# Kernel optimization log

Measured on AMD Instinct MI355X. Metric: run time of the kernel, lower is better.

Reference implementation:

```python
import jax, jax.numpy as jnp
import numpy as np

N_NODES = 100000
N_EDGES = 3200000
NUM_FEATURES = 5
HIDDEN = 64


def _gcn_layer(x, W, b, src, dst, norm, n_nodes):
    """One GCNConv: out = scatter_add(norm * (xW)[src] -> dst) + b.
    src/dst/norm already include self-loops and symmetric normalization."""
    h = x @ W                                  # [N, out_ch] small dense GEMM
    msg = h[src] * norm[:, None]               # [E+N, out_ch] gather + scale
    out = jax.ops.segment_sum(msg, dst, num_segments=n_nodes)
    return out + b


def _build_norm(edge_index, n_nodes):
    """Add self-loops, compute D^{-1/2}[src] * D^{-1/2}[dst] (GCN symmetric norm)."""
    loop = jnp.arange(n_nodes, dtype=edge_index.dtype)
    src = jnp.concatenate([edge_index[0], loop])
    dst = jnp.concatenate([edge_index[1], loop])
    deg = jax.ops.segment_sum(jnp.ones_like(dst, dtype=jnp.float32), dst,
                              num_segments=n_nodes)
    dis = jnp.where(deg > 0, jax.lax.rsqrt(deg), 0.0)  # deg^{-1/2}
    norm = dis[src] * dis[dst]
    return src, dst, norm


def setup_inputs() -> dict:
    key = jax.random.key(0)
    ks = jax.random.split(key, 8)
    x = jax.random.normal(ks[0], (N_NODES, NUM_FEATURES), dtype=jnp.float32)
    edge_index = jax.random.randint(ks[1], (2, N_EDGES), 0, N_NODES, dtype=jnp.int64)
    # glorot-ish scaled params
    W1 = jax.random.normal(ks[2], (NUM_FEATURES, HIDDEN), dtype=jnp.float32) * (1.0 / np.sqrt(NUM_FEATURES))
    b1 = jnp.zeros((HIDDEN,), dtype=jnp.float32)
    W2 = jax.random.normal(ks[3], (HIDDEN, HIDDEN), dtype=jnp.float32) * (1.0 / np.sqrt(HIDDEN))
    b2 = jnp.zeros((HIDDEN,), dtype=jnp.float32)
    W3 = jax.random.normal(ks[4], (HIDDEN, 1), dtype=jnp.float32) * (1.0 / np.sqrt(HIDDEN))
    b3 = jnp.zeros((1,), dtype=jnp.float32)
    return {"x": x, "edge_index": edge_index,
            "W1": W1, "b1": b1, "W2": W2, "b2": b2, "W3": W3, "b3": b3}


def reference(x, edge_index, W1, b1, W2, b2, W3, b3):
    n_nodes = x.shape[0]
    src, dst, norm = _build_norm(edge_index, n_nodes)
    h = jax.nn.relu(_gcn_layer(x, W1, b1, src, dst, norm, n_nodes))
    h = jax.nn.relu(_gcn_layer(h, W2, b2, src, dst, norm, n_nodes))
    out = _gcn_layer(h, W3, b3, src, dst, norm, n_nodes)  # [N, 1]
    return out
```

## Files before the change

kernel.cpp:

```cpp
#include <hip/hip_runtime.h>
#include <hip/hip_fp16.h>

#define NFEAT 5
#define HID 64
#define BSH 9
#define BNODES 512
#define MAXBK 256
#define PSH 14
#define NPART 8
#define CHUNK 4096

__global__ void k_zero(int* p, int n) {
    int i = blockIdx.x * blockDim.x + threadIdx.x;
    if (i < n) p[i] = 0;
}

__global__ __launch_bounds__(256) void
k_bhist(const int* __restrict__ dst, int* bhist, int E) {
    __shared__ int h[MAXBK];
    int t = threadIdx.x;
    h[t] = 0;
    __syncthreads();
    int i0 = blockIdx.x * CHUNK;
    int i1 = i0 + CHUNK; if (i1 > E) i1 = E;
    for (int i = i0 + t; i < i1; i += 256) atomicAdd(&h[dst[i] >> BSH], 1);
    __syncthreads();
    if (h[t]) atomicAdd(&bhist[t], h[t]);
}

__global__ void k_bscan(const int* __restrict__ bhist, int* bbase, int* bcur) {
    __shared__ int sh[MAXBK];
    int t = threadIdx.x;
    int v = bhist[t];
    sh[t] = v;
    __syncthreads();
    for (int off = 1; off < 256; off <<= 1) {
        int a = (t >= off) ? sh[t - off] : 0;
        __syncthreads();
        sh[t] += a;
        __syncthreads();
    }
    int excl = sh[t] - v;
    bbase[t] = excl;
    bcur[t]  = excl;
    if (t == 255) bbase[256] = sh[255];
}

__global__ __launch_bounds__(256) void
k_bin(const int* __restrict__ src, const int* __restrict__ dst,
      int* bcur, int2* __restrict__ binned, int E) {
    __shared__ int2 stg[CHUNK];
    __shared__ int hist[MAXBK], base[MAXBK], gb[MAXBK];
    int t = threadIdx.x;
    int e0 = blockIdx.x * CHUNK;
    int cc = E - e0; if (cc > CHUNK) cc = CHUNK;
    hist[t] = 0;
    __syncthreads();
    int2 my[CHUNK / 256]; int mb[CHUNK / 256];
#pragma unroll
    for (int k = 0; k < CHUNK / 256; ++k) {
        int i = e0 + k * 256 + t;
        if (i < E) {
            my[k].x = src[i]; my[k].y = dst[i];
            mb[k] = my[k].y >> BSH;
            atomicAdd(&hist[mb[k]], 1);
        } else mb[k] = -1;
    }
    __syncthreads();
    int c = hist[t];
    base[t] = c;
    __syncthreads();
    for (int off = 1; off < 256; off <<= 1) {
        int a = (t >= off) ? base[t - off] : 0;
        __syncthreads();
        base[t] += a;
        __syncthreads();
    }
    int excl = base[t] - c;
    base[t] = excl;
    gb[t] = c ? atomicAdd(&bcur[t], c) : 0;
    hist[t] = 0;
    __syncthreads();
#pragma unroll
    for (int k = 0; k < CHUNK / 256; ++k) {
        if (mb[k] >= 0) {
            int p = base[mb[k]] + atomicAdd(&hist[mb[k]], 1);
            stg[p] = my[k];
        }
    }
    __syncthreads();
#pragma unroll
    for (int k = 0; k < CHUNK / 256; ++k) {
        int p = k * 256 + t;
        if (p < cc) {
            int2 v = stg[p];
            int b = v.y >> BSH;
            binned[gb[b] + (p - base[b])] = v;
        }
    }
}

__global__ __launch_bounds__(256) void
k_sort(const int2* __restrict__ binned, const int* __restrict__ bbase,
       int* __restrict__ rpN, int* __restrict__ csr, float* __restrict__ dis,
       int n, int nbk) {
    __shared__ int hist[NPART * BNODES];
    __shared__ int cur[NPART * BNODES];
    __shared__ int tmp[256];
    int t = threadIdx.x, b = blockIdx.x;
    int e0 = bbase[b], e1 = bbase[b + 1];
    int v0 = b << BSH;
    int nv = n - v0; if (nv > BNODES) nv = BNODES;
#pragma unroll
    for (int k = 0; k < 16; ++k) hist[k * 256 + t] = 0;
    __syncthreads();
    for (int i = e0 + t; i < e1; i += 256) {
        int2 ed = binned[i];
        int bin = ((ed.y - v0) << 3) | (ed.x >> PSH);
        atomicAdd(&hist[bin], 1);
    }
    __syncthreads();
    for (int vl = t; vl < nv; vl += 256) {
        int d = 0;
#pragma unroll
        for (int p = 0; p < NPART; ++p) d += hist[(vl << 3) + p];
        dis[v0 + vl] = rsqrtf((float)d + 1.0f);
    }
    int s = 0, b0 = t * 16;
#pragma unroll
    for (int k = 0; k < 16; ++k) { cur[b0 + k] = s; s += hist[b0 + k]; }
    tmp[t] = s;
    __syncthreads();
    for (int off = 1; off < 256; off <<= 1) {
        int a = (t >= off) ? tmp[t - off] : 0;
        __syncthreads();
        tmp[t] += a;
        __syncthreads();
    }
    int add = e0 + tmp[t] - s;
#pragma unroll
    for (int k = 0; k < 16; ++k) cur[b0 + k] += add;
#pragma unroll
    for (int k = 0; k < 16; ++k) {
        int bin = b0 + k;
        if ((bin & 7) == 0) {
            int vl = bin >> 3;
            if (vl < nv) rpN[v0 + vl] = cur[bin];
        }
    }
    if (b == nbk - 1 && t == 0) rpN[n] = e1;
    __syncthreads();
    for (int i = e0 + t; i < e1; i += 256) {
        int2 ed = binned[i];
        int bin = ((ed.y - v0) << 3) | (ed.x >> PSH);
        int pos = atomicAdd(&cur[bin], 1);
        csr[pos] = ed.x;
    }
}

__global__ void k_xscale(const float* __restrict__ x, const float* __restrict__ dis,
                         float* __restrict__ xs, int n) {
    int i = blockIdx.x * blockDim.x + threadIdx.x;
    if (i >= n) return;
    float d = dis[i];
#pragma unroll
    for (int c = 0; c < NFEAT; ++c) xs[i * NFEAT + c] = d * x[i * NFEAT + c];
}

__global__ __launch_bounds__(256) void
k_layer1(const int* __restrict__ rpN, const int* __restrict__ csr,
         const float* __restrict__ xs, const float* __restrict__ dis,
         const float* __restrict__ W1, const float* __restrict__ b1,
         __half* __restrict__ g1h, int n) {
    int wave = (blockIdx.x * blockDim.x + threadIdx.x) >> 6;
    int lane = threadIdx.x & 63;
    if (wave >= n) return;
    int v = wave;
    int r0 = rpN[v], r1 = rpN[v + 1];
    float a0 = 0.f, a1 = 0.f, a2 = 0.f, a3 = 0.f, a4 = 0.f;
    for (int j = r0 + lane; j < r1; j += 64) {
        const float* p = xs + (size_t)csr[j] * NFEAT;
        a0 += p[0]; a1 += p[1]; a2 += p[2]; a3 += p[3]; a4 += p[4];
    }
#pragma unroll
    for (int m = 32; m > 0; m >>= 1) {
        a0 += __shfl_xor(a0, m, 64); a1 += __shfl_xor(a1, m, 64);
        a2 += __shfl_xor(a2, m, 64); a3 += __shfl_xor(a3, m, 64);
        a4 += __shfl_xor(a4, m, 64);
    }
    float dv = dis[v];
    const float* pv = xs + (size_t)v * NFEAT;
    a0 = dv * (a0 + pv[0]); a1 = dv * (a1 + pv[1]); a2 = dv * (a2 + pv[2]);
    a3 = dv * (a3 + pv[3]); a4 = dv * (a4 + pv[4]);
    int c = lane;
    float h = b1[c] + a0 * W1[c] + a1 * W1[64 + c] + a2 * W1[128 + c]
            + a3 * W1[192 + c] + a4 * W1[256 + c];
    g1h[(size_t)v * HID + c] = __float2half(dv * fmaxf(h, 0.0f));
}

__global__ __launch_bounds__(256) void
k_layer23(const int* __restrict__ rpN, const int* __restrict__ csr,
          const __half* __restrict__ g1h, const float* __restrict__ dis,
          const float* __restrict__ W2, const float* __restrict__ b2,
          const float* __restrict__ W3, float* __restrict__ svs, int n) {
    __shared__ float W2s[HID * HID];
    for (int i = threadIdx.x; i < HID * HID; i += 256) W2s[i] = W2[i];
    __syncthreads();
    int wave = (blockIdx.x * blockDim.x + threadIdx.x) >> 6;
    int lane = threadIdx.x & 63;
    if (wave >= n) return;
    int v = wave;
    int r0 = rpN[v], r1 = rpN[v + 1];
    float acc = __half2float(g1h[(size_t)v * HID + lane]);
    int j = r0;
    for (; j + 8 <= r1; j += 8) {
        int s0 = csr[j],     s1 = csr[j + 1], s2 = csr[j + 2], s3 = csr[j + 3];
        int s4 = csr[j + 4], s5 = csr[j + 5], s6 = csr[j + 6], s7 = csr[j + 7];
        float t0 = __half2float(g1h[(size_t)s0 * HID + lane]);
        float t1 = __half2float(g1h[(size_t)s1 * HID + lane]);
        float t2 = __half2float(g1h[(size_t)s2 * HID + lane]);
        float t3 = __half2float(g1h[(size_t)s3 * HID + lane]);
        float t4 = __half2float(g1h[(size_t)s4 * HID + lane]);
        float t5 = __half2float(g1h[(size_t)s5 * HID + lane]);
        float t6 = __half2float(g1h[(size_t)s6 * HID + lane]);
        float t7 = __half2float(g1h[(size_t)s7 * HID + lane]);
        acc += ((t0 + t1) + (t2 + t3)) + ((t4 + t5) + (t6 + t7));
    }
    for (; j < r1; ++j) acc += __half2float(g1h[(size_t)csr[j] * HID + lane]);
    float dv = dis[v];
    acc *= dv;
    float out = b2[lane];
#pragma unroll
    for (int k = 0; k < HID; ++k)
        out = fmaf(__shfl(acc, k, 64), W2s[(k << 6) + lane], out);
    out = fmaxf(out, 0.0f);
    float val = out * W3[lane];
#pragma unroll
    for (int m = 32; m > 0; m >>= 1) val += __shfl_xor(val, m, 64);
    if (lane == 0) svs[v] = dv * val;
}

__global__ __launch_bounds__(256) void
k_out(const int* __restrict__ rpN, const int* __restrict__ csr,
      const float* __restrict__ svs, const float* __restrict__ dis,
      const float* __restrict__ b3, float* __restrict__ out, int n) {
    int wave = (blockIdx.x * blockDim.x + threadIdx.x) >> 6;
    int lane = threadIdx.x & 63;
    if (wave >= n) return;
    int v = wave;
    int r0 = rpN[v], r1 = rpN[v + 1];
    float acc = (lane == 0) ? svs[v] : 0.f;
    for (int j = r0 + lane; j < r1; j += 64) acc += svs[csr[j]];
#pragma unroll
    for (int m = 32; m > 0; m >>= 1) acc += __shfl_xor(acc, m, 64);
    if (lane == 0) out[v] = b3[0] + dis[v] * acc;
}

extern "C" void kernel_launch(void* const* d_in, const int* in_sizes, int n_in,
                              void* d_out, int out_size, void* d_ws, size_t ws_size,
                              hipStream_t stream) {
    const float* x  = (const float*)d_in[0];
    const int*   ei = (const int*)d_in[1];
    const float* W1 = (const float*)d_in[2];
    const float* b1 = (const float*)d_in[3];
    const float* W2 = (const float*)d_in[4];
    const float* b2 = (const float*)d_in[5];
    const float* W3 = (const float*)d_in[6];
    const float* b3 = (const float*)d_in[7];
    float* out = (float*)d_out;

    const int n = out_size;
    const int E = in_sizes[1] / 2;
    const int* src = ei;
    const int* dst = ei + E;

    int*    bhist  = (int*)d_ws;
    int*    bbase  = bhist + 256;
    int*    bcur   = bhist + 520;
    int*    rpN    = bhist + 1024;
    float*  dis    = (float*)(rpN + n + 1);
    float*  svs    = dis + n;
    int*    csr    = (int*)(svs + n);
    int2*   binned = (int2*)(csr + E);
    __half* g1h    = (__half*)binned;
    float*  xs     = (float*)binned + (size_t)32 * n;

    const int B = 256;
    const int nchunk = (E + CHUNK - 1) / CHUNK;
    const int nbk    = (n + BNODES - 1) / BNODES;
    const int gridW  = ((size_t)n * 64 + B - 1) / B;

    k_zero   <<<1, 256, 0, stream>>>(bhist, 256);
    k_bhist  <<<nchunk, 256, 0, stream>>>(dst, bhist, E);
    k_bscan  <<<1, 256, 0, stream>>>(bhist, bbase, bcur);
    k_bin    <<<nchunk, 256, 0, stream>>>(src, dst, bcur, binned, E);
    k_sort   <<<nbk, 256, 0, stream>>>(binned, bbase, rpN, csr, dis, n, nbk);
    k_xscale <<<(n + B - 1) / B, B, 0, stream>>>(x, dis, xs, n);
    k_layer1 <<<gridW, B, 0, stream>>>(rpN, csr, xs, dis, W1, b1, g1h, n);
    k_layer23<<<gridW, B, 0, stream>>>(rpN, csr, g1h, dis, W2, b2, W3, svs, n);
    k_out    <<<gridW, B, 0, stream>>>(rpN, csr, svs, dis, b3, out, n);
}
```

Measured before the change: 418.9 us.

## Fuse x scaling into sort, drop source partitioning, pad xs to 8 floats

Removes the 8-way source-partition sub-binning in k_sort, so each node's edges are no longer grouped by source range. That shrinks shared memory and simplifies the scan, at the risk of worse gather locality in later layers. The k_xscale kernel is folded into k_sort, and xs is padded to 8 floats per node so layer1 can gather each row with two float4 loads. xs now sits after the binned buffer instead of overlapping it.

```diff
diff --git a/kernel.cpp b/kernel.cpp
--- a/kernel.cpp
+++ b/kernel.cpp
@@ -6,8 +6,6 @@
 #define BSH 9
 #define BNODES 512
 #define MAXBK 256
-#define PSH 14
-#define NPART 8
 #define CHUNK 4096
 
 __global__ void k_zero(int* p, int n) {
@@ -102,33 +100,35 @@
 
 __global__ __launch_bounds__(256) void
 k_sort(const int2* __restrict__ binned, const int* __restrict__ bbase,
-       int* __restrict__ rpN, int* __restrict__ csr, float* __restrict__ dis,
-       int n, int nbk) {
-    __shared__ int hist[NPART * BNODES];
-    __shared__ int cur[NPART * BNODES];
+       const float* __restrict__ x, int* __restrict__ rpN, int* __restrict__ csr,
+       float* __restrict__ dis, float* __restrict__ xs, int n, int nbk) {
+    __shared__ int hist[BNODES];
+    __shared__ int cur[BNODES];
     __shared__ int tmp[256];
     int t = threadIdx.x, b = blockIdx.x;
     int e0 = bbase[b], e1 = bbase[b + 1];
     int v0 = b << BSH;
     int nv = n - v0; if (nv > BNODES) nv = BNODES;
-#pragma unroll
-    for (int k = 0; k < 16; ++k) hist[k * 256 + t] = 0;
+    hist[t] = 0; hist[t + 256] = 0;
     __syncthreads();
     for (int i = e0 + t; i < e1; i += 256) {
         int2 ed = binned[i];
-        int bin = ((ed.y - v0) << 3) | (ed.x >> PSH);
-        atomicAdd(&hist[bin], 1);
+        atomicAdd(&hist[ed.y - v0], 1);
     }
     __syncthreads();
     for (int vl = t; vl < nv; vl += 256) {
-        int d = 0;
-#pragma unroll
-        for (int p = 0; p < NPART; ++p) d += hist[(vl << 3) + p];
-        dis[v0 + vl] = rsqrtf((float)d + 1.0f);
-    }
-    int s = 0, b0 = t * 16;
-#pragma unroll
-    for (int k = 0; k < 16; ++k) { cur[b0 + k] = s; s += hist[b0 + k]; }
+        int v = v0 + vl;
+        float dv = rsqrtf((float)hist[vl] + 1.0f);
+        dis[v] = dv;
+        const float* xr = x + (size_t)v * NFEAT;
+        float* xw = xs + (size_t)v * 8;
+        xw[0] = dv * xr[0]; xw[1] = dv * xr[1]; xw[2] = dv * xr[2];
+        xw[3] = dv * xr[3]; xw[4] = dv * xr[4];
+        xw[5] = 0.f; xw[6] = 0.f; xw[7] = 0.f;
+    }
+    int b0 = t * 2;
+    int c0 = hist[b0], c1 = hist[b0 + 1];
+    int s = c0 + c1;
     tmp[t] = s;
     __syncthreads();
     for (int off = 1; off < 256; off <<= 1) {
@@ -137,34 +137,18 @@
         tmp[t] += a;
         __syncthreads();
     }
-    int add = e0 + tmp[t] - s;
-#pragma unroll
-    for (int k = 0; k < 16; ++k) cur[b0 + k] += add;
-#pragma unroll
-    for (int k = 0; k < 16; ++k) {
-        int bin = b0 + k;
-        if ((bin & 7) == 0) {
-            int vl = bin >> 3;
-            if (vl < nv) rpN[v0 + vl] = cur[bin];
-        }
-    }
+    int excl = e0 + tmp[t] - s;
+    cur[b0] = excl;
+    cur[b0 + 1] = excl + c0;
+    if (b0 < nv)     rpN[v0 + b0]     = excl;
+    if (b0 + 1 < nv) rpN[v0 + b0 + 1] = excl + c0;
     if (b == nbk - 1 && t == 0) rpN[n] = e1;
     __syncthreads();
     for (int i = e0 + t; i < e1; i += 256) {
         int2 ed = binned[i];
-        int bin = ((ed.y - v0) << 3) | (ed.x >> PSH);
-        int pos = atomicAdd(&cur[bin], 1);
+        int pos = atomicAdd(&cur[ed.y - v0], 1);
         csr[pos] = ed.x;
     }
-}
-
-__global__ void k_xscale(const float* __restrict__ x, const float* __restrict__ dis,
-                         float* __restrict__ xs, int n) {
-    int i = blockIdx.x * blockDim.x + threadIdx.x;
-    if (i >= n) return;
-    float d = dis[i];
-#pragma unroll
-    for (int c = 0; c < NFEAT; ++c) xs[i * NFEAT + c] = d * x[i * NFEAT + c];
 }
 
 __global__ __launch_bounds__(256) void
@@ -179,8 +163,9 @@
     int r0 = rpN[v], r1 = rpN[v + 1];
     float a0 = 0.f, a1 = 0.f, a2 = 0.f, a3 = 0.f, a4 = 0.f;
     for (int j = r0 + lane; j < r1; j += 64) {
-        const float* p = xs + (size_t)csr[j] * NFEAT;
-        a0 += p[0]; a1 += p[1]; a2 += p[2]; a3 += p[3]; a4 += p[4];
+        const float4* q = (const float4*)(xs + (size_t)csr[j] * 8);
+        float4 qa = q[0], qb = q[1];
+        a0 += qa.x; a1 += qa.y; a2 += qa.z; a3 += qa.w; a4 += qb.x;
     }
 #pragma unroll
     for (int m = 32; m > 0; m >>= 1) {
@@ -189,7 +174,7 @@
         a4 += __shfl_xor(a4, m, 64);
     }
     float dv = dis[v];
-    const float* pv = xs + (size_t)v * NFEAT;
+    const float* pv = xs + (size_t)v * 8;
     a0 = dv * (a0 + pv[0]); a1 = dv * (a1 + pv[1]); a2 = dv * (a2 + pv[2]);
     a3 = dv * (a3 + pv[3]); a4 = dv * (a4 + pv[4]);
     int c = lane;
@@ -282,8 +267,8 @@
     float*  svs    = dis + n;
     int*    csr    = (int*)(svs + n);
     int2*   binned = (int2*)(csr + E);
+    float*  xs     = (float*)(binned + E);
     __half* g1h    = (__half*)binned;
-    float*  xs     = (float*)binned + (size_t)32 * n;
 
     const int B = 256;
     const int nchunk = (E + CHUNK - 1) / CHUNK;
@@ -294,8 +279,7 @@
     k_bhist  <<<nchunk, 256, 0, stream>>>(dst, bhist, E);
     k_bscan  <<<1, 256, 0, stream>>>(bhist, bbase, bcur);
     k_bin    <<<nchunk, 256, 0, stream>>>(src, dst, bcur, binned, E);
-    k_sort   <<<nbk, 256, 0, stream>>>(binned, bbase, rpN, csr, dis, n, nbk);
-    k_xscale <<<(n + B - 1) / B, B, 0, stream>>>(x, dis, xs, n);
+    k_sort   <<<nbk, 256, 0, stream>>>(binned, bbase, x, rpN, csr, dis, xs, n, nbk);
     k_layer1 <<<gridW, B, 0, stream>>>(rpN, csr, xs, dis, W1, b1, g1h, n);
     k_layer23<<<gridW, B, 0, stream>>>(rpN, csr, g1h, dis, W2, b2, W3, svs, n);
     k_out    <<<gridW, B, 0, stream>>>(rpN, csr, svs, dis, b3, out, n);
```

Measured after the change: 410.1 us. -2.1%, faster.
